# Optimization experiments

Measured on AMD Instinct MI355X. Metric: run time of the kernel, lower is better.

Reference implementation:

```python
import jax, jax.numpy as jnp
import numpy as np

# Module constants (match init_kwargs)
M = 2049                      # NpointsMesh (odd)
TAU = 2.821e-5                # Gaussian spreading width ~ 12*(pi/M)^2
XLIMS = (0.0, 10.0)
L = abs(XLIMS[1] - XLIMS[0])
KGRID = jnp.asarray(np.linspace(-(M // 2), M // 2, M), dtype=jnp.float32)        # (M,)
XGRID = jnp.asarray(2.0 * np.pi * np.linspace(XLIMS[0], XLIMS[1], M + 1)[:-1] / L,
                    dtype=jnp.float32)                                           # (M,)
FOUR_PI = 4.0 * np.pi


def setup_inputs() -> dict:
    key = jax.random.key(0)
    kx, = jax.random.split(key, 1)
    x = jax.random.uniform(kx, (16, 1024), dtype=jnp.float32) * 10.0  # points in [xLims[0], xLims[1])
    ones = jnp.ones((1,), dtype=jnp.float32)  # tf.initializers.ones for all 4 weights
    return {"x": x, "shift0": ones, "amp0": ones, "shift1": ones, "amp1": ones}


def reference(x, shift0, amp0, shift1, amp1):
    # Gaussian spreading: (B, N, M)
    diff = x[..., None] * (2.0 * np.pi / L) - XGRID
    g = jnp.exp(-jnp.square(diff) / (4.0 * TAU))
    # Sum over points -> gridded density (B, M), then FFT + shift
    gsum = jnp.sum(g, axis=1).astype(jnp.complex64)
    fft_g = jnp.fft.fftshift(jnp.fft.fft(gsum, axis=-1), axes=-1) * (L / (2.0 * np.pi))
    # Deconvolution of the Gaussian kernel (real-valued)
    deconv = jnp.sqrt(np.pi / TAU) * jnp.exp(jnp.square(KGRID) * TAU)  # (M,)
    rfft = fft_g * deconv  # (B, M) complex
    # Fourier multipliers (real; imag parts are structurally zero in the original)
    m1 = -amp0 * FOUR_PI / (jnp.square(KGRID) + jnp.square(5.0 * shift0))            # (M,)
    m2 = amp1 * FOUR_PI * jnp.square(1.0 / (jnp.square(KGRID) + jnp.square(5.0 * shift1)))  # (M,)
    mult = jnp.stack([m1, m2], axis=0)  # (2, M)
    mult_fft = mult[None, :, :].astype(jnp.complex64) * rfft[:, None, :]  # (B, 2, M)
    mult_deconv = mult_fft * deconv  # second deconv application, as in the original
    # Inverse FFT back to the mesh, keep real part: (B, 2, M)
    irfft = jnp.real(jnp.fft.ifft(jnp.fft.ifftshift(mult_deconv, axes=-1), axis=-1))
    # Inverse interpolation back to the points: (B, N, 2, M) -> (B, N, 2)
    local = irfft[:, None, :, :] * g[:, :, None, :]
    fmm = jnp.sum(local, axis=-1) / M
    return fmm
```

## Files before the change

kernel.cpp:

```cpp
#include <hip/hip_runtime.h>
#include <math.h>

#define M_   2049
#define B_   16
#define N_   1024
#define TAU_ 2.821e-5
#define PI_  3.14159265358979323846
#define TWO_PI_ 6.283185307179586476925286766559

#define GS_CH    8
#define H_JSPLIT 16
#define CV_SPLIT 16
#define FMM_LPP  16
#define MPAD     2052

#define SW(i) ((i) + ((i) >> 2))

__global__ void spread_h_kernel(const float* __restrict__ x,
                                const float* __restrict__ s0, const float* __restrict__ a0,
                                const float* __restrict__ s1, const float* __restrict__ a1,
                                double* __restrict__ gsum, double* __restrict__ hhalf) {
    __shared__ double smem[M_ + 128];
    const int bx = blockIdx.x;

    if (bx < GS_CH * B_) {
        const int b  = bx / GS_CH;
        const int ch = bx % GS_CH;
        for (int i = threadIdx.x; i < M_; i += 256) smem[i] = 0.0;
        __syncthreads();
        const int pl  = threadIdx.x >> 1;
        const int sub = threadIdx.x & 1;
        const double du      = TWO_PI_ / (double)M_;
        const double inv4tau = 1.0 / (4.0 * TAU_);
        const double u = (double)x[b * N_ + ch * (N_ / GS_CH) + pl] * (TWO_PI_ / 10.0);
        const int mc = (int)(u / du + 0.5);
        const int start = mc - 33 + sub * 34;
        for (int i = 0; i < 34; ++i) {
            int m = start + i;
            if (m >= 0 && m < M_) {
                double d = u - du * (double)m;
                double t = d * d * inv4tau;
                if (t < 88.0) atomicAdd(&smem[m], (double)__expf(-(float)t));
            }
        }
        __syncthreads();
        for (int i = threadIdx.x; i < M_; i += 256) {
            double v = smem[i];
            if (v != 0.0) atomicAdd(&gsum[b * M_ + i], v);
        }
    } else {
        const int t  = bx - GS_CH * B_;
        const int dt = t % 5;
        const int jc = t / 5;
        double* costab = smem;
        double* cf0    = smem + M_;
        double* cf1    = smem + M_ + 64;
        const int jlo = 1 + jc * (1024 / H_JSPLIT);
        const double ang0 = TWO_PI_ / (double)M_;

        for (int i = threadIdx.x; i <= 1024; i += 256) {
            double v = cos(ang0 * (double)i);
            costab[i] = v;
            if (i > 0) costab[M_ - i] = v;
        }
        if (threadIdx.x < 1024 / H_JSPLIT) {
            int j = jlo + threadIdx.x;
            double k2   = (double)j * (double)j;
            double dec2 = (PI_ / TAU_) * exp(2.0 * TAU_ * k2);
            double base = 2.0 * (10.0 / TWO_PI_) * dec2 / (double)M_;
            double sA = 5.0 * (double)s0[0];
            cf0[threadIdx.x] = base * (-(double)a0[0] * 4.0 * PI_ / (k2 + sA * sA));
            double sB = 5.0 * (double)s1[0];
            double den = k2 + sB * sB;
            cf1[threadIdx.x] = base * ((double)a1[0] * 4.0 * PI_ / (den * den));
        }
        __syncthreads();

        const int d = dt * 256 + threadIdx.x;
        if (d > 1024) return;

        double acc0 = 0.0, acc1 = 0.0;
        if (jc == 0) {
            double w0base = (10.0 / TWO_PI_) * (PI_ / TAU_) / (double)M_;
            double sA = 5.0 * (double)s0[0];
            acc0 = w0base * (-(double)a0[0] * 4.0 * PI_ / (sA * sA));
            double sB = 5.0 * (double)s1[0];
            acc1 = w0base * ((double)a1[0] * 4.0 * PI_ / ((sB * sB) * (sB * sB)));
        }
        int r = (int)(((long long)jlo * (long long)d) % M_);
        #pragma unroll 4
        for (int jj = 0; jj < 1024 / H_JSPLIT; ++jj) {
            double cv_ = costab[r];
            acc0 += cf0[jj] * cv_;
            acc1 += cf1[jj] * cv_;
            r += d; if (r >= M_) r -= M_;
        }
        atomicAdd(&hhalf[d], acc0);
        atomicAdd(&hhalf[1025 + d], acc1);
    }
}

__global__ void conv_kernel(const double* __restrict__ gsum, const double* __restrict__ hhalf,
                            double* __restrict__ part) {
    __shared__ double w0s[1456];
    __shared__ double w1s[1456];
    __shared__ double red[512];
    const int mt = blockIdx.x;
    const int s  = blockIdx.y;
    const int b  = blockIdx.z;
    const int m0  = mt * 1024;
    const int p0  = (s * M_) / CV_SPLIT;
    const int p1  = ((s + 1) * M_) / CV_SPLIT;
    const int len = p1 - p0;
    const int wcount = 1024 + len;
    int base = m0 - (p0 + len - 1);
    while (base < 0) base += M_;
    for (int i = threadIdx.x; i < wcount; i += 256) {
        int idx = base + i;
        while (idx >= M_) idx -= M_;
        int d = (idx > 1024) ? (M_ - idx) : idx;
        w0s[SW(i)] = hhalf[d];
        w1s[SW(i)] = hhalf[1025 + d];
    }
    __syncthreads();

    const double* gs = gsum + (size_t)b * M_ + p0;

    int q = 4 * threadIdx.x + len - 1;
    double c0w0 = w0s[SW(q)],   c0w1 = w0s[SW(q+1)], c0w2 = w0s[SW(q+2)], c0w3 = w0s[SW(q+3)];
    double c1w0 = w1s[SW(q)],   c1w1 = w1s[SW(q+1)], c1w2 = w1s[SW(q+2)], c1w3 = w1s[SW(q+3)];
    double a00 = 0.0, a01 = 0.0, a02 = 0.0, a03 = 0.0;
    double a10 = 0.0, a11 = 0.0, a12 = 0.0, a13 = 0.0;
    #pragma unroll 4
    for (int t = 0; t < len; ++t) {
        double g = gs[t];
        a00 += g * c0w0; a01 += g * c0w1; a02 += g * c0w2; a03 += g * c0w3;
        a10 += g * c1w0; a11 += g * c1w1; a12 += g * c1w2; a13 += g * c1w3;
        c0w3 = c0w2; c0w2 = c0w1; c0w1 = c0w0;
        c1w3 = c1w2; c1w2 = c1w1; c1w1 = c1w0;
        --q;
        c0w0 = w0s[SW(q)]; c1w0 = w1s[SW(q)];
    }
    {
        double* pv = part + (((size_t)s * B_ + b) * 2) * MPAD + m0 + 4 * threadIdx.x;
        pv[0]        = a00; pv[1]        = a01; pv[2]        = a02; pv[3]        = a03;
        pv[MPAD + 0] = a10; pv[MPAD + 1] = a11; pv[MPAD + 2] = a12; pv[MPAD + 3] = a13;
    }

    if (mt == 1) {
        double t0 = 0.0, t1 = 0.0;
        if (threadIdx.x < len) {
            double g = gs[threadIdx.x];
            int qq = 1023 + len - threadIdx.x;
            t0 = g * w0s[SW(qq)];
            t1 = g * w1s[SW(qq)];
        }
        red[threadIdx.x]       = t0;
        red[256 + threadIdx.x] = t1;
        __syncthreads();
        for (int off = 128; off > 0; off >>= 1) {
            if (threadIdx.x < off) {
                red[threadIdx.x]       += red[threadIdx.x + off];
                red[256 + threadIdx.x] += red[256 + threadIdx.x + off];
            }
            __syncthreads();
        }
        if (threadIdx.x == 0) {
            double* pv = part + (((size_t)s * B_ + b) * 2) * MPAD;
            pv[2048]        = red[0];
            pv[MPAD + 2048] = red[256];
        }
    }
}

__global__ void reduce_kernel(const double* __restrict__ part, double* __restrict__ conv) {
    const int idx = blockIdx.x * 256 + threadIdx.x;
    if (idx >= B_ * 2 * M_) return;
    const int b  = idx / (2 * M_);
    const int rm = idx - b * 2 * M_;
    const int c  = rm / M_;
    const int m  = rm - c * M_;
    const size_t off = ((size_t)b * 2 + c) * MPAD + m;
    const size_t sstride = (size_t)B_ * 2 * MPAD;
    double acc = 0.0;
    #pragma unroll
    for (int k = 0; k < CV_SPLIT; ++k)
        acc += part[(size_t)k * sstride + off];
    conv[idx] = acc;
}

__global__ void fmm_kernel(const float* __restrict__ x, const double* __restrict__ conv,
                           float* __restrict__ out) {
    const int gid = blockIdx.x * 256 + threadIdx.x;
    const int pt  = gid / FMM_LPP;
    const int sub = gid % FMM_LPP;
    const int b   = pt >> 10;
    const double du      = TWO_PI_ / (double)M_;
    const double inv4tau = 1.0 / (4.0 * TAU_);
    const double u = (double)x[pt] * (TWO_PI_ / 10.0);
    int mc = (int)(u / du + 0.5);
    int lo = mc - 34; if (lo < 0) lo = 0;
    int hi = mc + 34; if (hi > M_ - 1) hi = M_ - 1;
    const double* c0 = conv + (size_t)(b * 2) * M_;
    const double* c1 = c0 + M_;
    double a0 = 0.0, a1 = 0.0;
    for (int m = lo + sub; m <= hi; m += FMM_LPP) {
        double d = u - du * (double)m;
        double g = (double)__expf(-(float)(d * d * inv4tau));
        a0 += g * c0[m];
        a1 += g * c1[m];
    }
    a0 += __shfl_xor(a0, 1); a1 += __shfl_xor(a1, 1);
    a0 += __shfl_xor(a0, 2); a1 += __shfl_xor(a1, 2);
    a0 += __shfl_xor(a0, 4); a1 += __shfl_xor(a1, 4);
    a0 += __shfl_xor(a0, 8); a1 += __shfl_xor(a1, 8);
    if (sub == 0) {
        out[pt * 2 + 0] = (float)(a0 / (double)M_);
        out[pt * 2 + 1] = (float)(a1 / (double)M_);
    }
}

extern "C" void kernel_launch(void* const* d_in, const int* in_sizes, int n_in,
                              void* d_out, int out_size, void* d_ws, size_t ws_size,
                              hipStream_t stream) {
    (void)in_sizes; (void)n_in; (void)out_size; (void)ws_size;
    const float* x  = (const float*)d_in[0];
    const float* s0 = (const float*)d_in[1];
    const float* a0 = (const float*)d_in[2];
    const float* s1 = (const float*)d_in[3];
    const float* a1 = (const float*)d_in[4];
    float* out = (float*)d_out;

    double* gsum  = (double*)d_ws;
    double* hhalf = gsum + B_ * M_;
    double* conv  = hhalf + 2 * 1025;
    double* part  = conv + B_ * 2 * M_;

    hipMemsetAsync(d_ws, 0, (size_t)(B_ * M_ + 2 * 1025) * sizeof(double), stream);

    hipLaunchKernelGGL(spread_h_kernel, dim3(GS_CH * B_ + 5 * H_JSPLIT), dim3(256), 0,
                       stream, x, s0, a0, s1, a1, gsum, hhalf);
    hipLaunchKernelGGL(conv_kernel, dim3(2, CV_SPLIT, B_), dim3(256), 0, stream,
                       gsum, hhalf, part);
    hipLaunchKernelGGL(reduce_kernel, dim3((B_ * 2 * M_ + 255) / 256), dim3(256), 0, stream,
                       part, conv);
    hipLaunchKernelGGL(fmm_kernel, dim3(B_ * N_ * FMM_LPP / 256), dim3(256), 0, stream,
                       x, conv, out);
}
```

Measured before the change: 90.95 us.

## Fuse all stages into one cooperative persistent kernel with grid syncs

Replaces the memset and four separate launches with a single cooperative kernel of 512 blocks that separates the stages (spreading, kernel-coefficient synthesis, gsum reduction, convolution, partial reduction, interpolation) with grid.sync(). Atomic accumulation into global gsum and hhalf is replaced by per-chunk partial buffers followed by a deterministic reduction, and the cosine table lookup is replaced by a Chebyshev recurrence over all 1024 frequencies per thread. The aim is to cut launch and memset overhead and global atomics. In exchange it adds four grid-wide barriers and longer serial per-thread loops in the coefficient stage, and it depends on all 512 blocks being co-resident.

```diff
diff --git a/kernel.cpp b/kernel.cpp
--- a/kernel.cpp
+++ b/kernel.cpp
@@ -1,5 +1,8 @@
 #include <hip/hip_runtime.h>
+#include <hip/hip_cooperative_groups.h>
 #include <math.h>
+
+namespace cg = cooperative_groups;
 
 #define M_   2049
 #define B_   16
@@ -8,34 +11,41 @@
 #define PI_  3.14159265358979323846
 #define TWO_PI_ 6.283185307179586476925286766559
 
-#define GS_CH    8
-#define H_JSPLIT 16
+#define GS_CH    16
 #define CV_SPLIT 16
 #define FMM_LPP  16
 #define MPAD     2052
+#define NBLK     512
+#define NTHR     (NBLK * 256)
 
 #define SW(i) ((i) + ((i) >> 2))
 
-__global__ void spread_h_kernel(const float* __restrict__ x,
-                                const float* __restrict__ s0, const float* __restrict__ a0,
-                                const float* __restrict__ s1, const float* __restrict__ a1,
-                                double* __restrict__ gsum, double* __restrict__ hhalf) {
-    __shared__ double smem[M_ + 128];
-    const int bx = blockIdx.x;
+__global__ void __launch_bounds__(256, 2)
+mega_kernel(const float* __restrict__ x,
+            const float* __restrict__ s0, const float* __restrict__ a0,
+            const float* __restrict__ s1, const float* __restrict__ a1,
+            float* __restrict__ out,
+            double* __restrict__ gsum, double* __restrict__ hhalf,
+            double* __restrict__ part, double* __restrict__ gpart,
+            double* __restrict__ conv) {
+    cg::grid_group grid = cg::this_grid();
+    __shared__ double smem[3424];
+    const int bx  = blockIdx.x;
+    const int tid = threadIdx.x;
 
     if (bx < GS_CH * B_) {
-        const int b  = bx / GS_CH;
-        const int ch = bx % GS_CH;
-        for (int i = threadIdx.x; i < M_; i += 256) smem[i] = 0.0;
-        __syncthreads();
-        const int pl  = threadIdx.x >> 1;
-        const int sub = threadIdx.x & 1;
+        const int b  = bx >> 4;
+        const int ch = bx & 15;
+        for (int i = tid; i < M_; i += 256) smem[i] = 0.0;
+        __syncthreads();
+        const int pl  = tid >> 2;
+        const int sub = tid & 3;
         const double du      = TWO_PI_ / (double)M_;
         const double inv4tau = 1.0 / (4.0 * TAU_);
         const double u = (double)x[b * N_ + ch * (N_ / GS_CH) + pl] * (TWO_PI_ / 10.0);
         const int mc = (int)(u / du + 0.5);
-        const int start = mc - 33 + sub * 34;
-        for (int i = 0; i < 34; ++i) {
+        const int start = mc - 33 + sub * 17;
+        for (int i = 0; i < 17; ++i) {
             int m = start + i;
             if (m >= 0 && m < M_) {
                 double d = u - du * (double)m;
@@ -44,179 +54,180 @@
             }
         }
         __syncthreads();
-        for (int i = threadIdx.x; i < M_; i += 256) {
-            double v = smem[i];
-            if (v != 0.0) atomicAdd(&gsum[b * M_ + i], v);
-        }
-    } else {
-        const int t  = bx - GS_CH * B_;
-        const int dt = t % 5;
-        const int jc = t / 5;
-        double* costab = smem;
-        double* cf0    = smem + M_;
-        double* cf1    = smem + M_ + 64;
-        const int jlo = 1 + jc * (1024 / H_JSPLIT);
-        const double ang0 = TWO_PI_ / (double)M_;
-
-        for (int i = threadIdx.x; i <= 1024; i += 256) {
-            double v = cos(ang0 * (double)i);
-            costab[i] = v;
-            if (i > 0) costab[M_ - i] = v;
-        }
-        if (threadIdx.x < 1024 / H_JSPLIT) {
-            int j = jlo + threadIdx.x;
+        double* gp = gpart + ((size_t)ch * B_ + b) * M_;
+        for (int i = tid; i < M_; i += 256) gp[i] = smem[i];
+    } else if (bx < GS_CH * B_ + 5) {
+        const int dt = bx - GS_CH * B_;
+        double* cf0 = smem;
+        double* cf1 = smem + 1024;
+        const double sA = 5.0 * (double)s0[0];
+        const double sB = 5.0 * (double)s1[0];
+        const double A0 = -(double)a0[0] * 4.0 * PI_;
+        const double A1 =  (double)a1[0] * 4.0 * PI_;
+        for (int j = tid + 1; j <= 1024; j += 256) {
             double k2   = (double)j * (double)j;
             double dec2 = (PI_ / TAU_) * exp(2.0 * TAU_ * k2);
             double base = 2.0 * (10.0 / TWO_PI_) * dec2 / (double)M_;
-            double sA = 5.0 * (double)s0[0];
-            cf0[threadIdx.x] = base * (-(double)a0[0] * 4.0 * PI_ / (k2 + sA * sA));
-            double sB = 5.0 * (double)s1[0];
+            cf0[j - 1] = base * (A0 / (k2 + sA * sA));
             double den = k2 + sB * sB;
-            cf1[threadIdx.x] = base * ((double)a1[0] * 4.0 * PI_ / (den * den));
-        }
-        __syncthreads();
-
-        const int d = dt * 256 + threadIdx.x;
-        if (d > 1024) return;
-
-        double acc0 = 0.0, acc1 = 0.0;
-        if (jc == 0) {
-            double w0base = (10.0 / TWO_PI_) * (PI_ / TAU_) / (double)M_;
-            double sA = 5.0 * (double)s0[0];
-            acc0 = w0base * (-(double)a0[0] * 4.0 * PI_ / (sA * sA));
-            double sB = 5.0 * (double)s1[0];
-            acc1 = w0base * ((double)a1[0] * 4.0 * PI_ / ((sB * sB) * (sB * sB)));
-        }
-        int r = (int)(((long long)jlo * (long long)d) % M_);
+            cf1[j - 1] = base * (A1 / (den * den));
+        }
+        __syncthreads();
+        const int d = dt * 256 + tid;
+        if (d <= 1024) {
+            const double w0base = (10.0 / TWO_PI_) * (PI_ / TAU_) / (double)M_;
+            double acc0 = w0base * (A0 / (sA * sA));
+            double acc1 = w0base * (A1 / ((sB * sB) * (sB * sB)));
+            double c1    = cos(TWO_PI_ * (double)d / (double)M_);
+            double twoc1 = 2.0 * c1;
+            double cm1 = 1.0, c = c1;
+            #pragma unroll 4
+            for (int j = 1; j <= 1024; ++j) {
+                acc0 += cf0[j - 1] * c;
+                acc1 += cf1[j - 1] * c;
+                double cn = twoc1 * c - cm1;
+                cm1 = c; c = cn;
+            }
+            hhalf[d]        = acc0;
+            hhalf[1025 + d] = acc1;
+        }
+    }
+    grid.sync();
+
+    {
+        const int gid = bx * 256 + tid;
+        if (gid < B_ * M_) {
+            const size_t sstride = (size_t)B_ * M_;
+            double acc = 0.0;
+            #pragma unroll
+            for (int k = 0; k < GS_CH; ++k) acc += gpart[(size_t)k * sstride + gid];
+            gsum[gid] = acc;
+        }
+    }
+    grid.sync();
+
+    {
+        double* w0s = smem;
+        double* w1s = smem + 1456;
+        double* red = smem + 2912;
+        const int mt = bx & 1;
+        const int s  = (bx >> 1) & 15;
+        const int b  = bx >> 5;
+        const int m0  = mt * 1024;
+        const int p0  = (s * M_) / CV_SPLIT;
+        const int p1  = ((s + 1) * M_) / CV_SPLIT;
+        const int len = p1 - p0;
+        const int wcount = 1024 + len;
+        int base = m0 - (p0 + len - 1);
+        while (base < 0) base += M_;
+        for (int i = tid; i < wcount; i += 256) {
+            int idx = base + i;
+            while (idx >= M_) idx -= M_;
+            int d = (idx > 1024) ? (M_ - idx) : idx;
+            w0s[SW(i)] = hhalf[d];
+            w1s[SW(i)] = hhalf[1025 + d];
+        }
+        __syncthreads();
+
+        const double* gs = gsum + (size_t)b * M_ + p0;
+
+        int q = 4 * tid + len - 1;
+        double c0w0 = w0s[SW(q)],   c0w1 = w0s[SW(q+1)], c0w2 = w0s[SW(q+2)], c0w3 = w0s[SW(q+3)];
+        double c1w0 = w1s[SW(q)],   c1w1 = w1s[SW(q+1)], c1w2 = w1s[SW(q+2)], c1w3 = w1s[SW(q+3)];
+        double a00 = 0.0, a01 = 0.0, a02 = 0.0, a03 = 0.0;
+        double a10 = 0.0, a11 = 0.0, a12 = 0.0, a13 = 0.0;
         #pragma unroll 4
-        for (int jj = 0; jj < 1024 / H_JSPLIT; ++jj) {
-            double cv_ = costab[r];
-            acc0 += cf0[jj] * cv_;
-            acc1 += cf1[jj] * cv_;
-            r += d; if (r >= M_) r -= M_;
-        }
-        atomicAdd(&hhalf[d], acc0);
-        atomicAdd(&hhalf[1025 + d], acc1);
-    }
-}
-
-__global__ void conv_kernel(const double* __restrict__ gsum, const double* __restrict__ hhalf,
-                            double* __restrict__ part) {
-    __shared__ double w0s[1456];
-    __shared__ double w1s[1456];
-    __shared__ double red[512];
-    const int mt = blockIdx.x;
-    const int s  = blockIdx.y;
-    const int b  = blockIdx.z;
-    const int m0  = mt * 1024;
-    const int p0  = (s * M_) / CV_SPLIT;
-    const int p1  = ((s + 1) * M_) / CV_SPLIT;
-    const int len = p1 - p0;
-    const int wcount = 1024 + len;
-    int base = m0 - (p0 + len - 1);
-    while (base < 0) base += M_;
-    for (int i = threadIdx.x; i < wcount; i += 256) {
-        int idx = base + i;
-        while (idx >= M_) idx -= M_;
-        int d = (idx > 1024) ? (M_ - idx) : idx;
-        w0s[SW(i)] = hhalf[d];
-        w1s[SW(i)] = hhalf[1025 + d];
-    }
-    __syncthreads();
-
-    const double* gs = gsum + (size_t)b * M_ + p0;
-
-    int q = 4 * threadIdx.x + len - 1;
-    double c0w0 = w0s[SW(q)],   c0w1 = w0s[SW(q+1)], c0w2 = w0s[SW(q+2)], c0w3 = w0s[SW(q+3)];
-    double c1w0 = w1s[SW(q)],   c1w1 = w1s[SW(q+1)], c1w2 = w1s[SW(q+2)], c1w3 = w1s[SW(q+3)];
-    double a00 = 0.0, a01 = 0.0, a02 = 0.0, a03 = 0.0;
-    double a10 = 0.0, a11 = 0.0, a12 = 0.0, a13 = 0.0;
-    #pragma unroll 4
-    for (int t = 0; t < len; ++t) {
-        double g = gs[t];
-        a00 += g * c0w0; a01 += g * c0w1; a02 += g * c0w2; a03 += g * c0w3;
-        a10 += g * c1w0; a11 += g * c1w1; a12 += g * c1w2; a13 += g * c1w3;
-        c0w3 = c0w2; c0w2 = c0w1; c0w1 = c0w0;
-        c1w3 = c1w2; c1w2 = c1w1; c1w1 = c1w0;
-        --q;
-        c0w0 = w0s[SW(q)]; c1w0 = w1s[SW(q)];
-    }
-    {
-        double* pv = part + (((size_t)s * B_ + b) * 2) * MPAD + m0 + 4 * threadIdx.x;
-        pv[0]        = a00; pv[1]        = a01; pv[2]        = a02; pv[3]        = a03;
-        pv[MPAD + 0] = a10; pv[MPAD + 1] = a11; pv[MPAD + 2] = a12; pv[MPAD + 3] = a13;
-    }
-
-    if (mt == 1) {
-        double t0 = 0.0, t1 = 0.0;
-        if (threadIdx.x < len) {
-            double g = gs[threadIdx.x];
-            int qq = 1023 + len - threadIdx.x;
-            t0 = g * w0s[SW(qq)];
-            t1 = g * w1s[SW(qq)];
-        }
-        red[threadIdx.x]       = t0;
-        red[256 + threadIdx.x] = t1;
-        __syncthreads();
-        for (int off = 128; off > 0; off >>= 1) {
-            if (threadIdx.x < off) {
-                red[threadIdx.x]       += red[threadIdx.x + off];
-                red[256 + threadIdx.x] += red[256 + threadIdx.x + off];
-            }
+        for (int t = 0; t < len; ++t) {
+            double g = gs[t];
+            a00 += g * c0w0; a01 += g * c0w1; a02 += g * c0w2; a03 += g * c0w3;
+            a10 += g * c1w0; a11 += g * c1w1; a12 += g * c1w2; a13 += g * c1w3;
+            c0w3 = c0w2; c0w2 = c0w1; c0w1 = c0w0;
+            c1w3 = c1w2; c1w2 = c1w1; c1w1 = c1w0;
+            --q;
+            c0w0 = w0s[SW(q)]; c1w0 = w1s[SW(q)];
+        }
+        {
+            double* pv = part + (((size_t)s * B_ + b) * 2) * MPAD + m0 + 4 * tid;
+            pv[0]        = a00; pv[1]        = a01; pv[2]        = a02; pv[3]        = a03;
+            pv[MPAD + 0] = a10; pv[MPAD + 1] = a11; pv[MPAD + 2] = a12; pv[MPAD + 3] = a13;
+        }
+        if (mt == 1) {
+            double t0 = 0.0, t1 = 0.0;
+            if (tid < len) {
+                double g = gs[tid];
+                int qq = 1023 + len - tid;
+                t0 = g * w0s[SW(qq)];
+                t1 = g * w1s[SW(qq)];
+            }
+            red[tid]       = t0;
+            red[256 + tid] = t1;
             __syncthreads();
-        }
-        if (threadIdx.x == 0) {
-            double* pv = part + (((size_t)s * B_ + b) * 2) * MPAD;
-            pv[2048]        = red[0];
-            pv[MPAD + 2048] = red[256];
-        }
-    }
-}
-
-__global__ void reduce_kernel(const double* __restrict__ part, double* __restrict__ conv) {
-    const int idx = blockIdx.x * 256 + threadIdx.x;
-    if (idx >= B_ * 2 * M_) return;
-    const int b  = idx / (2 * M_);
-    const int rm = idx - b * 2 * M_;
-    const int c  = rm / M_;
-    const int m  = rm - c * M_;
-    const size_t off = ((size_t)b * 2 + c) * MPAD + m;
-    const size_t sstride = (size_t)B_ * 2 * MPAD;
-    double acc = 0.0;
-    #pragma unroll
-    for (int k = 0; k < CV_SPLIT; ++k)
-        acc += part[(size_t)k * sstride + off];
-    conv[idx] = acc;
-}
-
-__global__ void fmm_kernel(const float* __restrict__ x, const double* __restrict__ conv,
-                           float* __restrict__ out) {
-    const int gid = blockIdx.x * 256 + threadIdx.x;
-    const int pt  = gid / FMM_LPP;
-    const int sub = gid % FMM_LPP;
-    const int b   = pt >> 10;
-    const double du      = TWO_PI_ / (double)M_;
-    const double inv4tau = 1.0 / (4.0 * TAU_);
-    const double u = (double)x[pt] * (TWO_PI_ / 10.0);
-    int mc = (int)(u / du + 0.5);
-    int lo = mc - 34; if (lo < 0) lo = 0;
-    int hi = mc + 34; if (hi > M_ - 1) hi = M_ - 1;
-    const double* c0 = conv + (size_t)(b * 2) * M_;
-    const double* c1 = c0 + M_;
-    double a0 = 0.0, a1 = 0.0;
-    for (int m = lo + sub; m <= hi; m += FMM_LPP) {
-        double d = u - du * (double)m;
-        double g = (double)__expf(-(float)(d * d * inv4tau));
-        a0 += g * c0[m];
-        a1 += g * c1[m];
-    }
-    a0 += __shfl_xor(a0, 1); a1 += __shfl_xor(a1, 1);
-    a0 += __shfl_xor(a0, 2); a1 += __shfl_xor(a1, 2);
-    a0 += __shfl_xor(a0, 4); a1 += __shfl_xor(a1, 4);
-    a0 += __shfl_xor(a0, 8); a1 += __shfl_xor(a1, 8);
-    if (sub == 0) {
-        out[pt * 2 + 0] = (float)(a0 / (double)M_);
-        out[pt * 2 + 1] = (float)(a1 / (double)M_);
+            for (int off = 128; off > 0; off >>= 1) {
+                if (tid < off) {
+                    red[tid]       += red[tid + off];
+                    red[256 + tid] += red[256 + tid + off];
+                }
+                __syncthreads();
+            }
+            if (tid == 0) {
+                double* pv = part + (((size_t)s * B_ + b) * 2) * MPAD;
+                pv[2048]        = red[0];
+                pv[MPAD + 2048] = red[256];
+            }
+        }
+    }
+    grid.sync();
+
+    {
+        const int idx = bx * 256 + tid;
+        if (idx < B_ * 2 * M_) {
+            const int b  = idx / (2 * M_);
+            const int rm = idx - b * 2 * M_;
+            const int c  = rm / M_;
+            const int m  = rm - c * M_;
+            const size_t off = ((size_t)b * 2 + c) * MPAD + m;
+            const size_t sstride = (size_t)B_ * 2 * MPAD;
+            double acc = 0.0;
+            #pragma unroll
+            for (int k = 0; k < CV_SPLIT; ++k)
+                acc += part[(size_t)k * sstride + off];
+            conv[idx] = acc;
+        }
+    }
+    grid.sync();
+
+    {
+        const int gid = bx * 256 + tid;
+        const double du      = TWO_PI_ / (double)M_;
+        const double inv4tau = 1.0 / (4.0 * TAU_);
+        #pragma unroll
+        for (int it = 0; it < (B_ * N_ * FMM_LPP) / NTHR; ++it) {
+            const int unit = gid + it * NTHR;
+            const int pt  = unit / FMM_LPP;
+            const int sub = unit & (FMM_LPP - 1);
+            const int b   = pt >> 10;
+            const double u = (double)x[pt] * (TWO_PI_ / 10.0);
+            int mc = (int)(u / du + 0.5);
+            int lo = mc - 34; if (lo < 0) lo = 0;
+            int hi = mc + 34; if (hi > M_ - 1) hi = M_ - 1;
+            const double* c0 = conv + (size_t)(b * 2) * M_;
+            const double* c1 = c0 + M_;
+            double a0v = 0.0, a1v = 0.0;
+            for (int m = lo + sub; m <= hi; m += FMM_LPP) {
+                double d = u - du * (double)m;
+                double g = (double)__expf(-(float)(d * d * inv4tau));
+                a0v += g * c0[m];
+                a1v += g * c1[m];
+            }
+            a0v += __shfl_xor(a0v, 1); a1v += __shfl_xor(a1v, 1);
+            a0v += __shfl_xor(a0v, 2); a1v += __shfl_xor(a1v, 2);
+            a0v += __shfl_xor(a0v, 4); a1v += __shfl_xor(a1v, 4);
+            a0v += __shfl_xor(a0v, 8); a1v += __shfl_xor(a1v, 8);
+            if (sub == 0) {
+                out[pt * 2 + 0] = (float)(a0v / (double)M_);
+                out[pt * 2 + 1] = (float)(a1v / (double)M_);
+            }
+        }
     }
 }
 
@@ -235,15 +246,11 @@
     double* hhalf = gsum + B_ * M_;
     double* conv  = hhalf + 2 * 1025;
     double* part  = conv + B_ * 2 * M_;
-
-    hipMemsetAsync(d_ws, 0, (size_t)(B_ * M_ + 2 * 1025) * sizeof(double), stream);
-
-    hipLaunchKernelGGL(spread_h_kernel, dim3(GS_CH * B_ + 5 * H_JSPLIT), dim3(256), 0,
-                       stream, x, s0, a0, s1, a1, gsum, hhalf);
-    hipLaunchKernelGGL(conv_kernel, dim3(2, CV_SPLIT, B_), dim3(256), 0, stream,
-                       gsum, hhalf, part);
-    hipLaunchKernelGGL(reduce_kernel, dim3((B_ * 2 * M_ + 255) / 256), dim3(256), 0, stream,
-                       part, conv);
-    hipLaunchKernelGGL(fmm_kernel, dim3(B_ * N_ * FMM_LPP / 256), dim3(256), 0, stream,
-                       x, conv, out);
+    double* gpart = part + (size_t)CV_SPLIT * B_ * 2 * MPAD;
+
+    void* args[] = { (void*)&x, (void*)&s0, (void*)&a0, (void*)&s1, (void*)&a1,
+                     (void*)&out, (void*)&gsum, (void*)&hhalf, (void*)&part,
+                     (void*)&gpart, (void*)&conv };
+    hipLaunchCooperativeKernel((const void*)mega_kernel, dim3(NBLK), dim3(256),
+                               args, 0, stream);
 }
```

Measured after the change: 330.8 us. 3.64x slower.
